# Kernel optimization log

Hardware: AMD Instinct MI355X
Metric: run time of the kernel (lower is better)

Reference implementation:

```python
import jax, jax.numpy as jnp
import numpy as np
from jax import lax

B, C, CI, H, W_SP = 8, 64, 3, 224, 224  # batch, per-channel groups, in-chans per group, spatial
K, STRIDE = 5, 2


def setup_inputs() -> dict:
    key = jax.random.key(0)
    kx, kw = jax.random.split(key)
    x = jax.random.normal(kx, (B, C, CI, H, W_SP), dtype=jnp.float32)
    # one Conv2d(3->1, k=5, stride=2, bias=False) per output channel -> stacked [C, CI, K, K]
    fan_in = CI * K * K
    bound = 1.0 / np.sqrt(fan_in)
    W = jax.random.uniform(kw, (C, CI, K, K), dtype=jnp.float32, minval=-bound, maxval=bound)
    return {"x": x, "W": W}


def reference(x, W):
    # x: [B, C, CI, H, W]; each of the C groups has its own 3->1 conv (weights W[c]).
    # Equivalent to a single grouped conv: input [B, C*CI, H, W], feature_group_count=C.
    b, c, ci, h, w = x.shape
    x2 = x.reshape(b, c * ci, h, w)
    out = lax.conv_general_dilated(
        x2, W,
        window_strides=(STRIDE, STRIDE),
        padding="VALID",
        feature_group_count=c,
        dimension_numbers=("NCHW", "OIHW", "NCHW"),
    )  # [B, C, H_out, W_out]
    return out
```

## Files before the change

kernel.cpp:

```cpp
#include <hip/hip_runtime.h>

#define BATCH 8
#define CH 64
#define CIN 3
#define HIN 224
#define WIN 224
#define KSZ 5
#define STRIDE 2
#define HO 110
#define WO 110

#define TROWS 10
#define TILES (HO / TROWS)
#define NPLANES (BATCH * CH)
#define NWG (NPLANES * TILES)
#define INROWS (STRIDE * (TROWS - 1) + KSZ)
#define SLABF (INROWS * WIN)
#define SLABU (SLABF / 4)
#define TOTU (CIN * SLABU)
#define TPB 128
#define NITER ((TOTU + TPB - 1) / TPB)

typedef float float4a __attribute__((ext_vector_type(4)));
typedef float float2a __attribute__((ext_vector_type(2)));

#define GLOAD_LDS16(gsrc, ldsdst) \
    __builtin_amdgcn_global_load_lds((const __attribute__((address_space(1))) void*)(gsrc), \
                                     (__attribute__((address_space(3))) void*)(ldsdst), 16, 0, 0)

__global__ __launch_bounds__(TPB) void conv5_lds_kernel(
    const float* __restrict__ x,
    const float* __restrict__ Wt,
    float* __restrict__ out)
{
    __shared__ float xs[CIN * SLABF];
    __shared__ float wsh[CIN * KSZ * KSZ];

    const int wg  = blockIdx.x;
    const int per = NWG >> 3;
    const int swz = (wg & 7) * per + (wg >> 3);
    const int bc   = swz / TILES;
    const int tile = swz - bc * TILES;
    const int c = bc & (CH - 1);
    const int ho0 = tile * TROWS;
    const int ih0 = ho0 * STRIDE;

    const int tid = threadIdx.x;
    if (tid < CIN * KSZ * KSZ) {
        wsh[tid] = Wt[c * (CIN * KSZ * KSZ) + tid];
    }

    const char* gbase = (const char*)(x + (size_t)bc * (CIN * HIN * WIN));
#pragma unroll
    for (int k = 0; k < NITER; ++k) {
        const int u = k * TPB + tid;
        const int ci = (u >= 2 * SLABU) ? 2 : (u >= SLABU ? 1 : 0);
        const int rem = u - ci * SLABU;
        const char* src = gbase + (size_t)ci * (HIN * WIN * 4)
                                + (size_t)ih0 * (WIN * 4)
                                + (size_t)rem * 16;
        char* dst = (char*)xs + (size_t)(k * TPB + (tid & ~63)) * 16;
        if (u < TOTU) {
            GLOAD_LDS16(src, dst);
        }
    }

    __syncthreads();

    if (tid >= 110) return;
    const int px = tid % 55;
    const int ty = tid / 55;
    const int r0 = 10 * ty;

    float acc[5][2];
#pragma unroll
    for (int t = 0; t < 5; ++t) { acc[t][0] = 0.f; acc[t][1] = 0.f; }

#pragma unroll
    for (int ci = 0; ci < CIN; ++ci) {
        float wr[KSZ * KSZ];
#pragma unroll
        for (int i = 0; i < KSZ * KSZ; ++i) wr[i] = wsh[ci * KSZ * KSZ + i];

        const float* sp = xs + ci * SLABF + r0 * WIN + 4 * px;
#pragma unroll
        for (int rr = 0; rr < 13; ++rr) {
            float4a v0 = *(const float4a*)(sp + rr * WIN);
            float4a v1 = *(const float4a*)(sp + rr * WIN + 4);
            float xv[8] = {v0.x, v0.y, v0.z, v0.w, v1.x, v1.y, v1.z, v1.w};
#pragma unroll
            for (int t = 0; t < 5; ++t) {
                const int kh = rr - STRIDE * t;
                if (kh >= 0 && kh < KSZ) {
#pragma unroll
                    for (int kw = 0; kw < KSZ; ++kw) {
                        const float w = wr[kh * KSZ + kw];
                        acc[t][0] = fmaf(xv[kw],     w, acc[t][0]);
                        acc[t][1] = fmaf(xv[kw + 2], w, acc[t][1]);
                    }
                }
            }
        }
    }

    float* op = out + (size_t)bc * (HO * WO) + (size_t)(ho0 + 5 * ty) * WO + 2 * px;
#pragma unroll
    for (int t = 0; t < 5; ++t) {
        float2a v = {acc[t][0], acc[t][1]};
        *(float2a*)(op + (size_t)t * WO) = v;
    }
}

extern "C" void kernel_launch(void* const* d_in, const int* in_sizes, int n_in,
                              void* d_out, int out_size, void* d_ws, size_t ws_size,
                              hipStream_t stream)
{
    const float* x  = (const float*)d_in[0];
    const float* Wt = (const float*)d_in[1];
    float* out = (float*)d_out;

    conv5_lds_kernel<<<dim3(NWG), dim3(TPB), 0, stream>>>(x, Wt, out);
}
```

Before: 74.24 us.

## Use one persistent workgroup per plane with double-buffered slab pipeline

```diff
diff --git a/kernel.cpp b/kernel.cpp
--- a/kernel.cpp
+++ b/kernel.cpp
@@ -9,105 +9,122 @@
 #define STRIDE 2
 #define HO 110
 #define WO 110
+#define HW (HIN * WIN)
 
 #define TROWS 10
 #define TILES (HO / TROWS)
 #define NPLANES (BATCH * CH)
-#define NWG (NPLANES * TILES)
 #define INROWS (STRIDE * (TROWS - 1) + KSZ)
 #define SLABF (INROWS * WIN)
 #define SLABU (SLABF / 4)
-#define TOTU (CIN * SLABU)
 #define TPB 128
-#define NITER ((TOTU + TPB - 1) / TPB)
+#define NITER_S 11
+#define PADU (NITER_S * TPB)
+#define NSLAB (TILES * CIN)
 
 typedef float float4a __attribute__((ext_vector_type(4)));
 typedef float float2a __attribute__((ext_vector_type(2)));
 
-#define GLOAD_LDS16(gsrc, ldsdst) \
-    __builtin_amdgcn_global_load_lds((const __attribute__((address_space(1))) void*)(gsrc), \
-                                     (__attribute__((address_space(3))) void*)(ldsdst), 16, 0, 0)
+__device__ __forceinline__ void gload16(const float* src, float* ldsdst) {
+    __builtin_amdgcn_global_load_lds(
+        (const __attribute__((address_space(1))) void*)src,
+        (__attribute__((address_space(3))) void*)ldsdst, 16, 0, 0);
+}
 
-__global__ __launch_bounds__(TPB) void conv5_lds_kernel(
+__device__ __forceinline__ void stage_slab(const float* gplane, float* xbuf,
+                                           int sl, int tid) {
+    const int tile = sl / CIN;
+    const int ci = sl - CIN * tile;
+    const float* src0 = gplane + (size_t)ci * HW + (size_t)(tile * TROWS * STRIDE) * WIN;
+#pragma unroll
+    for (int k = 0; k < NITER_S; ++k) {
+        const int u = k * TPB + tid;
+        const int uc = (u < SLABU) ? u : (SLABU - 1);
+        gload16(src0 + (size_t)uc * 4, xbuf + (size_t)(k * TPB + (tid & ~63)) * 4);
+    }
+}
+
+__global__ __launch_bounds__(TPB) void conv5_pipe_kernel(
     const float* __restrict__ x,
     const float* __restrict__ Wt,
     float* __restrict__ out)
 {
-    __shared__ float xs[CIN * SLABF];
+    __shared__ float xs[2][PADU * 4];
     __shared__ float wsh[CIN * KSZ * KSZ];
 
-    const int wg  = blockIdx.x;
-    const int per = NWG >> 3;
-    const int swz = (wg & 7) * per + (wg >> 3);
-    const int bc   = swz / TILES;
-    const int tile = swz - bc * TILES;
+    const int bc = blockIdx.x;
     const int c = bc & (CH - 1);
-    const int ho0 = tile * TROWS;
-    const int ih0 = ho0 * STRIDE;
+    const int tid = threadIdx.x;
+    const float* gplane = x + (size_t)bc * (CIN * HW);
 
-    const int tid = threadIdx.x;
-    if (tid < CIN * KSZ * KSZ) {
-        wsh[tid] = Wt[c * (CIN * KSZ * KSZ) + tid];
-    }
-
-    const char* gbase = (const char*)(x + (size_t)bc * (CIN * HIN * WIN));
-#pragma unroll
-    for (int k = 0; k < NITER; ++k) {
-        const int u = k * TPB + tid;
-        const int ci = (u >= 2 * SLABU) ? 2 : (u >= SLABU ? 1 : 0);
-        const int rem = u - ci * SLABU;
-        const char* src = gbase + (size_t)ci * (HIN * WIN * 4)
-                                + (size_t)ih0 * (WIN * 4)
-                                + (size_t)rem * 16;
-        char* dst = (char*)xs + (size_t)(k * TPB + (tid & ~63)) * 16;
-        if (u < TOTU) {
-            GLOAD_LDS16(src, dst);
-        }
-    }
-
+    if (tid < CIN * KSZ * KSZ) wsh[tid] = Wt[c * (CIN * KSZ * KSZ) + tid];
     __syncthreads();
 
-    if (tid >= 110) return;
+    stage_slab(gplane, xs[0], 0, tid);
+    stage_slab(gplane, xs[1], 1, tid);
+
     const int px = tid % 55;
     const int ty = tid / 55;
-    const int r0 = 10 * ty;
 
     float acc[5][2];
 #pragma unroll
     for (int t = 0; t < 5; ++t) { acc[t][0] = 0.f; acc[t][1] = 0.f; }
 
+    for (int s = 0; s < NSLAB; ++s) {
+        if (s < NSLAB - 1) {
+            asm volatile("s_waitcnt vmcnt(11) lgkmcnt(0)" ::: "memory");
+        } else {
+            asm volatile("s_waitcnt vmcnt(0) lgkmcnt(0)" ::: "memory");
+        }
+        __builtin_amdgcn_s_barrier();
+        __builtin_amdgcn_sched_barrier(0);
+
+        const int tile = s / CIN;
+        const int ci = s - CIN * tile;
+
+        if (tid < 110) {
+            const float* wp = wsh + ci * (KSZ * KSZ);
+            float wr[KSZ * KSZ];
 #pragma unroll
-    for (int ci = 0; ci < CIN; ++ci) {
-        float wr[KSZ * KSZ];
+            for (int i = 0; i < KSZ * KSZ; ++i) wr[i] = wp[i];
+
+            const float* sp = xs[s & 1] + ty * (TROWS * WIN) + 4 * px;
 #pragma unroll
-        for (int i = 0; i < KSZ * KSZ; ++i) wr[i] = wsh[ci * KSZ * KSZ + i];
-
-        const float* sp = xs + ci * SLABF + r0 * WIN + 4 * px;
+            for (int rr = 0; rr < 13; ++rr) {
+                float4a v0 = *(const float4a*)(sp + rr * WIN);
+                float4a v1 = *(const float4a*)(sp + rr * WIN + 4);
+                float xv[8] = {v0.x, v0.y, v0.z, v0.w, v1.x, v1.y, v1.z, v1.w};
 #pragma unroll
-        for (int rr = 0; rr < 13; ++rr) {
-            float4a v0 = *(const float4a*)(sp + rr * WIN);
-            float4a v1 = *(const float4a*)(sp + rr * WIN + 4);
-            float xv[8] = {v0.x, v0.y, v0.z, v0.w, v1.x, v1.y, v1.z, v1.w};
+                for (int t = 0; t < 5; ++t) {
+                    const int kh = rr - STRIDE * t;
+                    if (kh >= 0 && kh < KSZ) {
 #pragma unroll
-            for (int t = 0; t < 5; ++t) {
-                const int kh = rr - STRIDE * t;
-                if (kh >= 0 && kh < KSZ) {
-#pragma unroll
-                    for (int kw = 0; kw < KSZ; ++kw) {
-                        const float w = wr[kh * KSZ + kw];
-                        acc[t][0] = fmaf(xv[kw],     w, acc[t][0]);
-                        acc[t][1] = fmaf(xv[kw + 2], w, acc[t][1]);
+                        for (int kw = 0; kw < KSZ; ++kw) {
+                            const float w = wr[kh * KSZ + kw];
+                            acc[t][0] = fmaf(xv[kw],     w, acc[t][0]);
+                            acc[t][1] = fmaf(xv[kw + 2], w, acc[t][1]);
+                        }
                     }
                 }
             }
+
+            if (ci == CIN - 1) {
+                float* op = out + (size_t)bc * (HO * WO)
+                                + (size_t)(tile * TROWS + 5 * ty) * WO + 2 * px;
+#pragma unroll
+                for (int t = 0; t < 5; ++t) {
+                    float2a v = {acc[t][0], acc[t][1]};
+                    *(float2a*)(op + (size_t)t * WO) = v;
+                    acc[t][0] = 0.f; acc[t][1] = 0.f;
+                }
+            }
         }
-    }
 
-    float* op = out + (size_t)bc * (HO * WO) + (size_t)(ho0 + 5 * ty) * WO + 2 * px;
-#pragma unroll
-    for (int t = 0; t < 5; ++t) {
-        float2a v = {acc[t][0], acc[t][1]};
-        *(float2a*)(op + (size_t)t * WO) = v;
+        asm volatile("s_waitcnt lgkmcnt(0)" ::: "memory");
+        __builtin_amdgcn_s_barrier();
+        __builtin_amdgcn_sched_barrier(0);
+
+        if (s + 2 < NSLAB) stage_slab(gplane, xs[s & 1], s + 2, tid);
     }
 }
 
@@ -119,5 +136,5 @@
     const float* Wt = (const float*)d_in[1];
     float* out = (float*)d_out;
 
-    conv5_lds_kernel<<<dim3(NWG), dim3(TPB), 0, stream>>>(x, Wt, out);
+    conv5_pipe_kernel<<<dim3(NPLANES), dim3(TPB), 0, stream>>>(x, Wt, out);
 }
```

New measurement: 72.43 us. 1.02x faster.
